# Performance work log

Hardware: AMD Instinct MI355X
Metric: run time of the kernel (lower is better)

Reference implementation:

```python
import jax, jax.numpy as jnp
import numpy as np

B, S, T = 1024, 512, 64
NEG = -10000.0


def setup_inputs() -> dict:
    key = jax.random.key(0)
    k1, k2 = jax.random.split(key)
    feats = jax.random.normal(k1, (B, S, T), dtype=jnp.float32)
    transitions = jax.random.normal(k2, (T, T), dtype=jnp.float32)
    # reset_parameters: transitions[START_IDX, :] = -10000 ; transitions[:, END_IDX] = -10000
    transitions = transitions.at[T - 2, :].set(NEG).at[:, T - 1].set(NEG)
    return {"feats": feats, "transitions": transitions}


def reference(feats, transitions):
    """Batched Viterbi decode: returns (path_score [B], best_path [B, S] int32)."""
    b, s, t = feats.shape
    START = t - 2
    END = t - 1

    init = jnp.full((b, t), NEG, dtype=feats.dtype).at[:, START].set(0.0)

    def step(forward_var, feat):
        # next_tag_var[b, next, prev] = forward_var[b, prev] + transitions[next, prev]
        next_tag_var = forward_var[:, None, :] + transitions[None, :, :]
        viterbivars = jnp.max(next_tag_var, axis=2)          # [B, T]
        bptrs = jnp.argmax(next_tag_var, axis=2)             # [B, T]
        return viterbivars + feat, bptrs

    feats_t = jnp.swapaxes(feats, 0, 1)                      # [S, B, T]
    forward_var, backpointers = jax.lax.scan(step, init, feats_t)  # bps: [S, B, T]

    terminal_var = forward_var + transitions[END]            # [B, T]
    path_score = jnp.max(terminal_var, axis=1)               # [B]
    best_tag = jnp.argmax(terminal_var, axis=1)              # [B]

    def backtrace(tag, bptrs_t):
        # emit tag at this position, then follow backpointer
        prev_tag = jnp.take_along_axis(bptrs_t, tag[:, None], axis=1)[:, 0]
        return prev_tag, tag

    # reverse scan: ys[i] = decoded tag at position i
    _, tags = jax.lax.scan(backtrace, best_tag, backpointers, reverse=True)  # [S, B]
    best_path = tags.T.astype(jnp.int32)                     # [B, S]
    return path_score, best_path
```

## Files before the change

kernel.cpp:

```cpp
#include <hip/hip_runtime.h>


#define B_ 1024
#define S_ 512
#define T_ 64
#define NEGV -10000.0f

__global__ __launch_bounds__(64, 1) void viterbi_fwd_bt(
    const float* __restrict__ feats,
    const float* __restrict__ trans,
    float* __restrict__ out,
    float* __restrict__ vv)
{
    __shared__ float T_lds[T_ * T_];
    __shared__ __align__(16) float fvbuf[2][T_];

    const int b = blockIdx.x;
    const int lane = threadIdx.x;

    {
        const float4* src = reinterpret_cast<const float4*>(trans);
        float4* dst = reinterpret_cast<float4*>(T_lds);
#pragma unroll
        for (int i = 0; i < 16; ++i) dst[i * 64 + lane] = src[i * 64 + lane];
    }

    float t[T_];
#pragma unroll
    for (int p = 0; p < T_; p += 4) {
        const float4 v = *reinterpret_cast<const float4*>(trans + lane * T_ + p);
        t[p] = v.x; t[p + 1] = v.y; t[p + 2] = v.z; t[p + 3] = v.w;
    }
    const float tend = trans[(T_ - 1) * T_ + lane];

    float fv = (lane == T_ - 2) ? 0.0f : NEGV;
    fvbuf[0][lane] = fv;

    const float* fb = feats + (size_t)b * S_ * T_ + lane;
    float* vw = vv + (size_t)b * S_ * T_ + lane;

    float fc[4], fn[4];
#pragma unroll
    for (int k = 0; k < 4; ++k) fc[k] = fb[(size_t)k * T_];

#pragma unroll 1
    for (int s4 = 0; s4 < S_ / 4; ++s4) {
#pragma unroll
        for (int k = 0; k < 4; ++k) {
            int sp = 4 * s4 + 4 + k;
            sp = (sp < S_) ? sp : (S_ - 1);
            fn[k] = fb[(size_t)sp * T_];
        }
#pragma unroll
        for (int u = 0; u < 4; ++u) {
            const int s = 4 * s4 + u;
            const int rs = s & 1;
            float gm[16];
#pragma unroll
            for (int j = 0; j < 16; ++j) {
                const float4 v = *reinterpret_cast<const float4*>(&fvbuf[rs][4 * j]);
                const float c0 = v.x + t[4 * j + 0];
                const float c1 = v.y + t[4 * j + 1];
                const float c2 = v.z + t[4 * j + 2];
                const float c3 = v.w + t[4 * j + 3];
                gm[j] = fmaxf(fmaxf(c0, c1), fmaxf(c2, c3));
            }
#pragma unroll
            for (int off = 8; off >= 1; off >>= 1)
#pragma unroll
                for (int j = 0; j < off; ++j) gm[j] = fmaxf(gm[j], gm[j + off]);
            const float maxv = gm[0];

            vw[(size_t)s * T_] = maxv;
            fv = maxv + fc[u];
            fvbuf[rs ^ 1][lane] = fv;
        }
#pragma unroll
        for (int k = 0; k < 4; ++k) fc[k] = fn[k];
    }

    float v = fv + tend;
    int i = lane;
#pragma unroll
    for (int off = 1; off < 64; off <<= 1) {
        const float vo = __shfl_xor(v, off);
        const int io = __shfl_xor(i, off);
        const bool take = (vo > v) || ((vo == v) && (io < i));
        v = take ? vo : v;
        i = take ? io : i;
    }
    int ncur = __builtin_amdgcn_readfirstlane(i);
    if (lane == 0) out[b] = v;

    asm volatile("s_waitcnt vmcnt(0)" ::: "memory");

    float A = vw[(size_t)(S_ - 1) * T_];
    float vvR[8], ffR[8];
#pragma unroll
    for (int k = 0; k < 8; ++k) {
        const int s = (S_ - 1) - k;
        vvR[k] = vw[(size_t)(s - 1) * T_];
        ffR[k] = fb[(size_t)(s - 1) * T_];
    }

    float emitv = 0.0f;
    float* outp = out + B_ + (size_t)b * S_;

#pragma unroll 1
    for (int c = 7; c >= 0; --c) {
#pragma unroll 1
        for (int g = 7; g >= 0; --g) {
            const int base = 64 * c + 8 * g;
#pragma unroll
            for (int kk = 0; kk < 8; ++kk) {
                const int s = base + 7 - kk;
                emitv = (lane == (s & 63)) ? (float)ncur : emitv;
                if (s > 0) {
                    const float target = __int_as_float(
                        __builtin_amdgcn_readlane(__float_as_int(A), ncur));
                    const float trow = T_lds[(ncur << 6) + lane];
                    const float cand = (vvR[kk] + ffR[kk]) + trow;
                    const unsigned long long m = __ballot(cand == target);
                    ncur = ((int)__builtin_ctzll(m)) & 63;
                    A = vvR[kk];
                    const int sp = (s >= 9) ? (s - 9) : 0;
                    vvR[kk] = vw[(size_t)sp * T_];
                    ffR[kk] = fb[(size_t)sp * T_];
                }
            }
        }
        outp[64 * c + lane] = emitv;
    }
}

__global__ __launch_bounds__(64, 1) void viterbi_kernel(
    const float* __restrict__ feats,
    const float* __restrict__ trans,
    float* __restrict__ out)
{
    __shared__ unsigned int bp[S_ / 4][T_];
    __shared__ __align__(16) float fvbuf[2][T_];

    const int b = blockIdx.x;
    const int lane = threadIdx.x;

    float t[T_];
#pragma unroll
    for (int p = 0; p < T_; p += 4) {
        const float4 v = *reinterpret_cast<const float4*>(trans + lane * T_ + p);
        t[p] = v.x; t[p + 1] = v.y; t[p + 2] = v.z; t[p + 3] = v.w;
    }
    const float tend = trans[(T_ - 1) * T_ + lane];

    float fv = (lane == T_ - 2) ? 0.0f : NEGV;
    fvbuf[0][lane] = fv;

    const float* fb = feats + (size_t)b * S_ * T_ + lane;

    float fc[4], fn[4];
#pragma unroll
    for (int k = 0; k < 4; ++k) fc[k] = fb[(size_t)k * T_];

#pragma unroll 1
    for (int s4 = 0; s4 < S_ / 4; ++s4) {
#pragma unroll
        for (int k = 0; k < 4; ++k) {
            int sp = 4 * s4 + 4 + k;
            sp = (sp < S_) ? sp : (S_ - 1);
            fn[k] = fb[(size_t)sp * T_];
        }

        unsigned int pack = 0;
#pragma unroll
        for (int u = 0; u < 4; ++u) {
            const int s = 4 * s4 + u;
            const int rs = s & 1;

            float fvl[T_];
#pragma unroll
            for (int j = 0; j < 16; ++j) {
                const float4 v = *reinterpret_cast<const float4*>(&fvbuf[rs][4 * j]);
                fvl[4 * j] = v.x; fvl[4 * j + 1] = v.y;
                fvl[4 * j + 2] = v.z; fvl[4 * j + 3] = v.w;
            }

            float bv[4]; int bi[4];
#pragma unroll
            for (int g = 0; g < 4; ++g) {
                float bestv = fvl[16 * g] + t[16 * g];
                int besti = 16 * g;
#pragma unroll
                for (int q = 1; q < 16; ++q) {
                    const int p = 16 * g + q;
                    const float c = fvl[p] + t[p];
                    const bool gt = c > bestv;
                    besti = gt ? p : besti;
                    bestv = gt ? c : bestv;
                }
                bv[g] = bestv; bi[g] = besti;
            }
            float BV = bv[0]; int BI = bi[0];
#pragma unroll
            for (int g = 1; g < 4; ++g) {
                const bool gt = bv[g] > BV;
                BI = gt ? bi[g] : BI;
                BV = gt ? bv[g] : BV;
            }

            fv = BV + fc[u];
            fvbuf[rs ^ 1][lane] = fv;
            pack |= ((unsigned int)BI) << (8 * u);
        }
        bp[s4][lane] = pack;

#pragma unroll
        for (int k = 0; k < 4; ++k) fc[k] = fn[k];
    }

    float v = fv + tend;
    int i = lane;
#pragma unroll
    for (int off = 1; off < 64; off <<= 1) {
        const float vo = __shfl_xor(v, off);
        const int io = __shfl_xor(i, off);
        const bool take = (vo > v) || ((vo == v) && (io < i));
        v = take ? vo : v;
        i = take ? io : i;
    }
    int tcur = __builtin_amdgcn_readfirstlane(i);
    if (lane == 0) out[b] = v;

    float* outp = out + B_ + (size_t)b * S_;
#pragma unroll 1
    for (int c = 7; c >= 0; --c) {
        unsigned int wd[16];
#pragma unroll
        for (int j = 0; j < 16; ++j)
            wd[j] = bp[16 * c + j][lane];

        int emit = 0;
#pragma unroll
        for (int k = 63; k >= 0; --k) {
            emit = (lane == k) ? tcur : emit;
            const int word = __builtin_amdgcn_readlane((int)wd[k >> 2], tcur);
            tcur = (word >> (8 * (k & 3))) & 0xff;
        }
        outp[64 * c + lane] = (float)emit;
    }
}

extern "C" void kernel_launch(void* const* d_in, const int* in_sizes, int n_in,
                              void* d_out, int out_size, void* d_ws, size_t ws_size,
                              hipStream_t stream) {
    const float* feats = (const float*)d_in[0];
    const float* trans = (const float*)d_in[1];
    float* out = (float*)d_out;

    const size_t need = (size_t)B_ * S_ * T_ * sizeof(float);
    if (d_ws != nullptr && ws_size >= need) {
        viterbi_fwd_bt<<<dim3(B_), dim3(T_), 0, stream>>>(feats, trans, out, (float*)d_ws);
    } else {
        viterbi_kernel<<<dim3(B_), dim3(T_), 0, stream>>>(feats, trans, out);
    }
}
```

Measured before the change: 329.6 us.

## Split max-plus step across 8-lane groups with packed adds and DPP reductions

```diff
diff --git a/kernel.cpp b/kernel.cpp
--- a/kernel.cpp
+++ b/kernel.cpp
@@ -1,10 +1,22 @@
 #include <hip/hip_runtime.h>
 
+
+typedef float v2f __attribute__((ext_vector_type(2)));
 
 #define B_ 1024
 #define S_ 512
 #define T_ 64
 #define NEGV -10000.0f
+
+#define DPP_XOR1 0xB1
+#define DPP_XOR2 0x4E
+#define DPP_HMIRR 0x141
+
+template <int CTRL>
+__device__ __forceinline__ float dppmax(float x) {
+    const int y = __builtin_amdgcn_update_dpp(0, __float_as_int(x), CTRL, 0xf, 0xf, true);
+    return fmaxf(x, __int_as_float(y));
+}
 
 __global__ __launch_bounds__(64, 1) void viterbi_fwd_bt(
     const float* __restrict__ feats,
@@ -17,6 +29,8 @@
 
     const int b = blockIdx.x;
     const int lane = threadIdx.x;
+    const int gn = lane >> 3;
+    const int gp = lane & 7;
 
     {
         const float4* src = reinterpret_cast<const float4*>(trans);
@@ -25,13 +39,20 @@
         for (int i = 0; i < 16; ++i) dst[i * 64 + lane] = src[i * 64 + lane];
     }
 
-    float t[T_];
-#pragma unroll
-    for (int p = 0; p < T_; p += 4) {
-        const float4 v = *reinterpret_cast<const float4*>(trans + lane * T_ + p);
-        t[p] = v.x; t[p + 1] = v.y; t[p + 2] = v.z; t[p + 3] = v.w;
+    v2f T8[8][4];
+#pragma unroll
+    for (int i = 0; i < 8; ++i) {
+        const float* r = trans + (8 * gn + i) * T_ + 8 * gp;
+        const float4 u0 = *reinterpret_cast<const float4*>(r);
+        const float4 u1 = *reinterpret_cast<const float4*>(r + 4);
+        T8[i][0] = v2f{u0.x, u0.y}; T8[i][1] = v2f{u0.z, u0.w};
+        T8[i][2] = v2f{u1.x, u1.y}; T8[i][3] = v2f{u1.z, u1.w};
     }
     const float tend = trans[(T_ - 1) * T_ + lane];
+
+    const bool s0 = (lane & 1) != 0;
+    const bool s1 = (lane & 2) != 0;
+    const bool s2 = (lane & 4) != 0;
 
     float fv = (lane == T_ - 2) ? 0.0f : NEGV;
     fvbuf[0][lane] = fv;
@@ -55,21 +76,39 @@
         for (int u = 0; u < 4; ++u) {
             const int s = 4 * s4 + u;
             const int rs = s & 1;
-            float gm[16];
-#pragma unroll
-            for (int j = 0; j < 16; ++j) {
-                const float4 v = *reinterpret_cast<const float4*>(&fvbuf[rs][4 * j]);
-                const float c0 = v.x + t[4 * j + 0];
-                const float c1 = v.y + t[4 * j + 1];
-                const float c2 = v.z + t[4 * j + 2];
-                const float c3 = v.w + t[4 * j + 3];
-                gm[j] = fmaxf(fmaxf(c0, c1), fmaxf(c2, c3));
-            }
-#pragma unroll
-            for (int off = 8; off >= 1; off >>= 1)
-#pragma unroll
-                for (int j = 0; j < off; ++j) gm[j] = fmaxf(gm[j], gm[j + off]);
-            const float maxv = gm[0];
+
+            const float4 a0 = *reinterpret_cast<const float4*>(&fvbuf[rs][8 * gp]);
+            const float4 a1 = *reinterpret_cast<const float4*>(&fvbuf[rs][8 * gp + 4]);
+            const v2f f0 = v2f{a0.x, a0.y}, f1 = v2f{a0.z, a0.w};
+            const v2f f2 = v2f{a1.x, a1.y}, f3 = v2f{a1.z, a1.w};
+
+            float m[8];
+#pragma unroll
+            for (int i = 0; i < 8; ++i) {
+                const v2f c0 = f0 + T8[i][0];
+                const v2f c1 = f1 + T8[i][1];
+                const v2f c2 = f2 + T8[i][2];
+                const v2f c3 = f3 + T8[i][3];
+                const float x = fmaxf(fmaxf(c0.x, c0.y), c1.x);
+                const float y = fmaxf(fmaxf(c1.y, c2.x), c2.y);
+                const float z = fmaxf(c3.x, c3.y);
+                m[i] = fmaxf(fmaxf(x, y), z);
+            }
+
+#pragma unroll
+            for (int i = 0; i < 8; ++i) m[i] = dppmax<DPP_XOR1>(m[i]);
+#pragma unroll
+            for (int i = 0; i < 8; ++i) m[i] = dppmax<DPP_XOR2>(m[i]);
+#pragma unroll
+            for (int i = 0; i < 8; ++i) m[i] = dppmax<DPP_HMIRR>(m[i]);
+
+            const float x0 = s0 ? m[1] : m[0];
+            const float x1 = s0 ? m[3] : m[2];
+            const float x2 = s0 ? m[5] : m[4];
+            const float x3 = s0 ? m[7] : m[6];
+            const float y0 = s1 ? x1 : x0;
+            const float y1 = s1 ? x3 : x2;
+            const float maxv = s2 ? y1 : y0;
 
             vw[(size_t)s * T_] = maxv;
             fv = maxv + fc[u];
@@ -120,8 +159,8 @@
                         __builtin_amdgcn_readlane(__float_as_int(A), ncur));
                     const float trow = T_lds[(ncur << 6) + lane];
                     const float cand = (vvR[kk] + ffR[kk]) + trow;
-                    const unsigned long long m = __ballot(cand == target);
-                    ncur = ((int)__builtin_ctzll(m)) & 63;
+                    const unsigned long long msk = __ballot(cand == target);
+                    ncur = ((int)__builtin_ctzll(msk)) & 63;
                     A = vvR[kk];
                     const int sp = (s >= 9) ? (s - 9) : 0;
                     vvR[kk] = vw[(size_t)sp * T_];
```

Result: slower. 356.4 us (+8.1%).

## Process two batch rows per wavefront in forward Viterbi with packed float2 adds

Applied to the files above, without the earlier changes.

```diff
diff --git a/kernel.cpp b/kernel.cpp
--- a/kernel.cpp
+++ b/kernel.cpp
@@ -1,21 +1,24 @@
 #include <hip/hip_runtime.h>
 
+
+typedef float v2f __attribute__((ext_vector_type(2)));
 
 #define B_ 1024
 #define S_ 512
 #define T_ 64
 #define NEGV -10000.0f
 
-__global__ __launch_bounds__(64, 1) void viterbi_fwd_bt(
+__global__ __launch_bounds__(64, 1) void viterbi_fwd_bt2(
     const float* __restrict__ feats,
     const float* __restrict__ trans,
     float* __restrict__ out,
     float* __restrict__ vv)
 {
     __shared__ float T_lds[T_ * T_];
-    __shared__ __align__(16) float fvbuf[2][T_];
-
-    const int b = blockIdx.x;
+    __shared__ __align__(16) float fvbuf[2][2][T_];
+
+    const int b0 = blockIdx.x * 2;
+    const int b1 = b0 + 1;
     const int lane = threadIdx.x;
 
     {
@@ -25,23 +28,31 @@
         for (int i = 0; i < 16; ++i) dst[i * 64 + lane] = src[i * 64 + lane];
     }
 
-    float t[T_];
+    v2f t2[32];
 #pragma unroll
     for (int p = 0; p < T_; p += 4) {
         const float4 v = *reinterpret_cast<const float4*>(trans + lane * T_ + p);
-        t[p] = v.x; t[p + 1] = v.y; t[p + 2] = v.z; t[p + 3] = v.w;
+        t2[p / 2] = v2f{v.x, v.y};
+        t2[p / 2 + 1] = v2f{v.z, v.w};
     }
     const float tend = trans[(T_ - 1) * T_ + lane];
 
-    float fv = (lane == T_ - 2) ? 0.0f : NEGV;
-    fvbuf[0][lane] = fv;
-
-    const float* fb = feats + (size_t)b * S_ * T_ + lane;
-    float* vw = vv + (size_t)b * S_ * T_ + lane;
-
-    float fc[4], fn[4];
-#pragma unroll
-    for (int k = 0; k < 4; ++k) fc[k] = fb[(size_t)k * T_];
+    float fv0 = (lane == T_ - 2) ? 0.0f : NEGV;
+    float fv1 = fv0;
+    fvbuf[0][0][lane] = fv0;
+    fvbuf[1][0][lane] = fv1;
+
+    const float* fb0 = feats + (size_t)b0 * S_ * T_ + lane;
+    const float* fb1 = feats + (size_t)b1 * S_ * T_ + lane;
+    float* vw0 = vv + (size_t)b0 * S_ * T_ + lane;
+    float* vw1 = vv + (size_t)b1 * S_ * T_ + lane;
+
+    float fc0[4], fn0[4], fc1[4], fn1[4];
+#pragma unroll
+    for (int k = 0; k < 4; ++k) {
+        fc0[k] = fb0[(size_t)k * T_];
+        fc1[k] = fb1[(size_t)k * T_];
+    }
 
 #pragma unroll 1
     for (int s4 = 0; s4 < S_ / 4; ++s4) {
@@ -49,87 +60,147 @@
         for (int k = 0; k < 4; ++k) {
             int sp = 4 * s4 + 4 + k;
             sp = (sp < S_) ? sp : (S_ - 1);
-            fn[k] = fb[(size_t)sp * T_];
+            fn0[k] = fb0[(size_t)sp * T_];
+            fn1[k] = fb1[(size_t)sp * T_];
         }
 #pragma unroll
         for (int u = 0; u < 4; ++u) {
             const int s = 4 * s4 + u;
             const int rs = s & 1;
-            float gm[16];
+
+            float g0[16];
 #pragma unroll
             for (int j = 0; j < 16; ++j) {
-                const float4 v = *reinterpret_cast<const float4*>(&fvbuf[rs][4 * j]);
-                const float c0 = v.x + t[4 * j + 0];
-                const float c1 = v.y + t[4 * j + 1];
-                const float c2 = v.z + t[4 * j + 2];
-                const float c3 = v.w + t[4 * j + 3];
-                gm[j] = fmaxf(fmaxf(c0, c1), fmaxf(c2, c3));
-            }
-#pragma unroll
-            for (int off = 8; off >= 1; off >>= 1)
-#pragma unroll
-                for (int j = 0; j < off; ++j) gm[j] = fmaxf(gm[j], gm[j + off]);
-            const float maxv = gm[0];
-
-            vw[(size_t)s * T_] = maxv;
-            fv = maxv + fc[u];
-            fvbuf[rs ^ 1][lane] = fv;
-        }
-#pragma unroll
-        for (int k = 0; k < 4; ++k) fc[k] = fn[k];
-    }
-
-    float v = fv + tend;
-    int i = lane;
+                const float4 q = *reinterpret_cast<const float4*>(&fvbuf[0][rs][4 * j]);
+                const v2f a = v2f{q.x, q.y} + t2[2 * j];
+                const v2f c = v2f{q.z, q.w} + t2[2 * j + 1];
+                g0[j] = fmaxf(fmaxf(a.x, a.y), fmaxf(c.x, c.y));
+            }
+            float g1[16];
+#pragma unroll
+            for (int j = 0; j < 16; ++j) {
+                const float4 q = *reinterpret_cast<const float4*>(&fvbuf[1][rs][4 * j]);
+                const v2f a = v2f{q.x, q.y} + t2[2 * j];
+                const v2f c = v2f{q.z, q.w} + t2[2 * j + 1];
+                g1[j] = fmaxf(fmaxf(a.x, a.y), fmaxf(c.x, c.y));
+            }
+#pragma unroll
+            for (int off = 8; off >= 1; off >>= 1) {
+#pragma unroll
+                for (int j = 0; j < off; ++j) {
+                    g0[j] = fmaxf(g0[j], g0[j + off]);
+                    g1[j] = fmaxf(g1[j], g1[j + off]);
+                }
+            }
+            const float maxv0 = g0[0];
+            const float maxv1 = g1[0];
+
+            vw0[(size_t)s * T_] = maxv0;
+            vw1[(size_t)s * T_] = maxv1;
+            fv0 = maxv0 + fc0[u];
+            fv1 = maxv1 + fc1[u];
+            fvbuf[0][rs ^ 1][lane] = fv0;
+            fvbuf[1][rs ^ 1][lane] = fv1;
+        }
+#pragma unroll
+        for (int k = 0; k < 4; ++k) { fc0[k] = fn0[k]; fc1[k] = fn1[k]; }
+    }
+
+    float v0 = fv0 + tend, v1 = fv1 + tend;
+    int i0 = lane, i1 = lane;
 #pragma unroll
     for (int off = 1; off < 64; off <<= 1) {
-        const float vo = __shfl_xor(v, off);
-        const int io = __shfl_xor(i, off);
-        const bool take = (vo > v) || ((vo == v) && (io < i));
-        v = take ? vo : v;
-        i = take ? io : i;
-    }
-    int ncur = __builtin_amdgcn_readfirstlane(i);
-    if (lane == 0) out[b] = v;
+        const float vo0 = __shfl_xor(v0, off);
+        const int io0 = __shfl_xor(i0, off);
+        const float vo1 = __shfl_xor(v1, off);
+        const int io1 = __shfl_xor(i1, off);
+        const bool t0 = (vo0 > v0) || ((vo0 == v0) && (io0 < i0));
+        const bool t1 = (vo1 > v1) || ((vo1 == v1) && (io1 < i1));
+        v0 = t0 ? vo0 : v0; i0 = t0 ? io0 : i0;
+        v1 = t1 ? vo1 : v1; i1 = t1 ? io1 : i1;
+    }
+    int ncur0 = __builtin_amdgcn_readfirstlane(i0);
+    int ncur1 = __builtin_amdgcn_readfirstlane(i1);
+    if (lane == 0) { out[b0] = v0; out[b1] = v1; }
 
     asm volatile("s_waitcnt vmcnt(0)" ::: "memory");
 
-    float A = vw[(size_t)(S_ - 1) * T_];
-    float vvR[8], ffR[8];
-#pragma unroll
-    for (int k = 0; k < 8; ++k) {
-        const int s = (S_ - 1) - k;
-        vvR[k] = vw[(size_t)(s - 1) * T_];
-        ffR[k] = fb[(size_t)(s - 1) * T_];
-    }
-
-    float emitv = 0.0f;
-    float* outp = out + B_ + (size_t)b * S_;
-
-#pragma unroll 1
-    for (int c = 7; c >= 0; --c) {
-#pragma unroll 1
-        for (int g = 7; g >= 0; --g) {
-            const int base = 64 * c + 8 * g;
-#pragma unroll
-            for (int kk = 0; kk < 8; ++kk) {
-                const int s = base + 7 - kk;
-                emitv = (lane == (s & 63)) ? (float)ncur : emitv;
-                if (s > 0) {
-                    const float target = __int_as_float(
-                        __builtin_amdgcn_readlane(__float_as_int(A), ncur));
-                    const float trow = T_lds[(ncur << 6) + lane];
-                    const float cand = (vvR[kk] + ffR[kk]) + trow;
-                    const unsigned long long m = __ballot(cand == target);
-                    ncur = ((int)__builtin_ctzll(m)) & 63;
-                    A = vvR[kk];
-                    const int sp = (s >= 9) ? (s - 9) : 0;
-                    vvR[kk] = vw[(size_t)sp * T_];
-                    ffR[kk] = fb[(size_t)sp * T_];
+    {
+        float A = vw0[(size_t)(S_ - 1) * T_];
+        float vvR[8], ffR[8];
+#pragma unroll
+        for (int k = 0; k < 8; ++k) {
+            const int s = (S_ - 1) - k;
+            vvR[k] = vw0[(size_t)(s - 1) * T_];
+            ffR[k] = fb0[(size_t)(s - 1) * T_];
+        }
+        float emitv = 0.0f;
+        float* outp = out + B_ + (size_t)b0 * S_;
+        int ncur = ncur0;
+#pragma unroll 1
+        for (int c = 7; c >= 0; --c) {
+#pragma unroll 1
+            for (int g = 7; g >= 0; --g) {
+                const int base = 64 * c + 8 * g;
+#pragma unroll
+                for (int kk = 0; kk < 8; ++kk) {
+                    const int s = base + 7 - kk;
+                    emitv = (lane == (s & 63)) ? (float)ncur : emitv;
+                    if (s > 0) {
+                        const float target = __int_as_float(
+                            __builtin_amdgcn_readlane(__float_as_int(A), ncur));
+                        const float trow = T_lds[(ncur << 6) + lane];
+                        const float cand = (vvR[kk] + ffR[kk]) + trow;
+                        const unsigned long long m = __ballot(cand == target);
+                        ncur = ((int)__builtin_ctzll(m)) & 63;
+                        A = vvR[kk];
+                        const int sp = (s >= 9) ? (s - 9) : 0;
+                        vvR[kk] = vw0[(size_t)sp * T_];
+                        ffR[kk] = fb0[(size_t)sp * T_];
+                    }
                 }
             }
-        }
-        outp[64 * c + lane] = emitv;
+            outp[64 * c + lane] = emitv;
+        }
+    }
+
+    {
+        float A = vw1[(size_t)(S_ - 1) * T_];
+        float vvR[8], ffR[8];
+#pragma unroll
+        for (int k = 0; k < 8; ++k) {
+            const int s = (S_ - 1) - k;
+            vvR[k] = vw1[(size_t)(s - 1) * T_];
+            ffR[k] = fb1[(size_t)(s - 1) * T_];
+        }
+        float emitv = 0.0f;
+        float* outp = out + B_ + (size_t)b1 * S_;
+        int ncur = ncur1;
+#pragma unroll 1
+        for (int c = 7; c >= 0; --c) {
+#pragma unroll 1
+            for (int g = 7; g >= 0; --g) {
+                const int base = 64 * c + 8 * g;
+#pragma unroll
+                for (int kk = 0; kk < 8; ++kk) {
+                    const int s = base + 7 - kk;
+                    emitv = (lane == (s & 63)) ? (float)ncur : emitv;
+                    if (s > 0) {
+                        const float target = __int_as_float(
+                            __builtin_amdgcn_readlane(__float_as_int(A), ncur));
+                        const float trow = T_lds[(ncur << 6) + lane];
+                        const float cand = (vvR[kk] + ffR[kk]) + trow;
+                        const unsigned long long m = __ballot(cand == target);
+                        ncur = ((int)__builtin_ctzll(m)) & 63;
+                        A = vvR[kk];
+                        const int sp = (s >= 9) ? (s - 9) : 0;
+                        vvR[kk] = vw1[(size_t)sp * T_];
+                        ffR[kk] = fb1[(size_t)sp * T_];
+                    }
+                }
+            }
+            outp[64 * c + lane] = emitv;
+        }
     }
 }
 
@@ -258,7 +329,7 @@
 
     const size_t need = (size_t)B_ * S_ * T_ * sizeof(float);
     if (d_ws != nullptr && ws_size >= need) {
-        viterbi_fwd_bt<<<dim3(B_), dim3(T_), 0, stream>>>(feats, trans, out, (float*)d_ws);
+        viterbi_fwd_bt2<<<dim3(B_ / 2), dim3(T_), 0, stream>>>(feats, trans, out, (float*)d_ws);
     } else {
         viterbi_kernel<<<dim3(B_), dim3(T_), 0, stream>>>(feats, trans, out);
     }
```

New measurement: 782.1 us. +137.3%, slower.
